# Optimization experiments

Hardware: AMD Instinct MI355X
Metric: run time of the kernel (lower is better)

## Reference

```python
import jax, jax.numpy as jnp
import numpy as np

NUM_HEADS = 16
EMBED_DIM = 1024
LN_EPS = 1e-5


def setup_inputs() -> dict:
    key = jax.random.key(0)
    ks = jax.random.split(key, 9)
    B, S, D = 4, 1024, EMBED_DIM
    return {
        "query": jax.random.normal(ks[0], (B, S, D), dtype=jnp.float32),
        "key": jax.random.normal(ks[1], (B, S, D), dtype=jnp.float32),
        "value": jax.random.normal(ks[2], (B, S, D), dtype=jnp.float32),
        "W_query": 0.01 * jax.random.normal(ks[3], (D, D), dtype=jnp.float32),
        "W_key": 0.01 * jax.random.normal(ks[4], (D, D), dtype=jnp.float32),
        "W_value": 0.01 * jax.random.normal(ks[5], (D, D), dtype=jnp.float32),
        "W_output": 0.01 * jax.random.normal(ks[6], (D, D), dtype=jnp.float32),
        "ln_gamma": jnp.ones((D,), dtype=jnp.float32),
        "ln_beta": jnp.zeros((D,), dtype=jnp.float32),
        "mask": 1,
    }


def _split_heads(x):
    # [B,S,D] -> [H,B,S,d]; torch split(dim=-1)+stack(dim=0) gives head h = cols h*d:(h+1)*d
    B, S, D = x.shape
    d = D // NUM_HEADS
    return jnp.moveaxis(x.reshape(B, S, NUM_HEADS, d), 2, 0)


def reference(query, key, value, W_query, W_key, W_value, W_output, ln_gamma, ln_beta, mask):
    B, S, D = query.shape
    d = D // NUM_HEADS
    q = _split_heads(query @ W_query)   # [H,B,S,d]
    k = _split_heads(key @ W_key)       # [H,B,S,d]
    v = _split_heads(value @ W_value)   # [H,B,S,d]
    scale = jnp.asarray(np.sqrt(d), dtype=q.dtype)
    scores = jnp.einsum("hbqd,hbkd->hbqk", q, k) / scale  # [H,B,S,S]
    attn = jax.nn.softmax(scores, axis=-1)
    if mask:
        # post-hoc causal: zero strict upper triangle, then renormalize rows
        tri = jnp.tril(jnp.ones((S, S), dtype=bool))
        attn = jnp.where(tri, attn, 0.0)
        attn = attn / jnp.sum(attn, axis=-1, keepdims=True)
    ws = jnp.einsum("hbqk,hbkd->hbqd", attn, v)            # [H,B,S,d]
    concat = jnp.moveaxis(ws, 0, 2).reshape(B, S, D)       # [B,S,D]
    out = concat @ W_output + query                        # residual
    mu = jnp.mean(out, axis=-1, keepdims=True)
    var = jnp.var(out, axis=-1, keepdims=True)
    out = (out - mu) / jnp.sqrt(var + LN_EPS) * ln_gamma + ln_beta
    return out, attn
```

## Files before the change

kernel.cpp:

```cpp
#include <hip/hip_runtime.h>
#include <hip/hip_bf16.h>

#define Bn   4
#define Sn   1024
#define Dn   1024
#define Hn   16
#define dHn  64
#define HB   (Hn * Bn)
#define MROWS (Bn * Sn)
#define QNE  ((size_t)Bn * Sn * Dn)

typedef __attribute__((ext_vector_type(8))) short bf16x8;
typedef __attribute__((ext_vector_type(4))) float f32x4;

__device__ __forceinline__ ushort f2bf(float x) {
  union { float f; unsigned u; } v; v.f = x;
  unsigned r = v.u + 0x7FFF + ((v.u >> 16) & 1);
  return (ushort)(r >> 16);
}
__device__ __forceinline__ float bf2f(ushort u) {
  union { unsigned u; float f; } v; v.u = ((unsigned)u) << 16; return v.f;
}

__device__ __forceinline__ void load_lds16(const void* g, void* l) {
  __builtin_amdgcn_global_load_lds(
      (const __attribute__((address_space(1))) unsigned int*)g,
      (__attribute__((address_space(3))) unsigned int*)l, 16, 0, 0);
}

__global__ __launch_bounds__(256) void cast3_kernel(
    const float* __restrict__ q, const float* __restrict__ k,
    const float* __restrict__ v, ushort* __restrict__ outb) {
  const float* in = blockIdx.y == 0 ? q : (blockIdx.y == 1 ? k : v);
  ushort* out = outb + (size_t)blockIdx.y * QNE;
  int idx = blockIdx.x * 256 + threadIdx.x;
  float4 x = *(const float4*)&in[(size_t)idx * 4];
  ushort4 o;
  o.x = f2bf(x.x); o.y = f2bf(x.y); o.z = f2bf(x.z); o.w = f2bf(x.w);
  *(ushort4*)&out[(size_t)idx * 4] = o;
}

__global__ __launch_bounds__(256) void transpose4_kernel(
    const float* __restrict__ Wq, const float* __restrict__ Wk,
    const float* __restrict__ Wv, const float* __restrict__ Wo,
    ushort* __restrict__ WTb) {
  const int z = blockIdx.z;
  const float* W = z == 0 ? Wq : (z == 1 ? Wk : (z == 2 ? Wv : Wo));
  ushort* WT = WTb + (size_t)z * Dn * Dn;
  __shared__ ushort T[64 * 72];
  const int k0 = blockIdx.y * 64, n0 = blockIdx.x * 64;
  const int t = threadIdx.x;
  const int r = t >> 4, c4 = (t & 15) * 4;
#pragma unroll
  for (int i = 0; i < 4; ++i) {
    int row = r + i * 16;
    float4 v = *(const float4*)&W[(size_t)(k0 + row) * Dn + n0 + c4];
    T[(c4 + 0) * 72 + row] = f2bf(v.x);
    T[(c4 + 1) * 72 + row] = f2bf(v.y);
    T[(c4 + 2) * 72 + row] = f2bf(v.z);
    T[(c4 + 3) * 72 + row] = f2bf(v.w);
  }
  __syncthreads();
#pragma unroll
  for (int i = 0; i < 2; ++i) {
    int c = t + i * 256;
    int n = c >> 3, kg = (c & 7) * 8;
    *(ulonglong2*)&WT[(size_t)(n0 + n) * Dn + k0 + kg] =
        *(const ulonglong2*)&T[n * 72 + kg];
  }
}

__global__ __launch_bounds__(256, 3) void qkv_gemm(
    const ushort* __restrict__ Ab, const ushort* __restrict__ Bb,
    ushort* __restrict__ Cb) {
  const int z = blockIdx.z;
  const ushort* A  = Ab + (size_t)z * QNE;
  const ushort* Bt = Bb + (size_t)z * Dn * Dn;
  ushort* C        = Cb + (size_t)z * QNE;
  const int N = Dn, K = Dn;

  __shared__ ushort lds[17408];
  ushort* As = lds;
  ushort* Bs = lds + 4096;
  const int t = threadIdx.x;
  const int w = t >> 6, lane = t & 63;
  const int wr = (w >> 1) * 64, wc = (w & 1) * 64;
  const int l16 = lane & 15, quad = lane >> 4;
  const int flat = blockIdx.y * 8 + blockIdx.x;
  const int nf = (flat & 7) * 32 + (flat >> 3);
  const int m0 = (nf >> 3) * 128, n0 = (nf & 7) * 128;
  const int srow = (lane >> 2);
  const int scol = (lane & 3) * 8;
  f32x4 acc[4][4] = {};
  for (int k0 = 0; k0 < K; k0 += 32) {
#pragma unroll
    for (int c = 0; c < 2; ++c) {
      int row = w * 32 + c * 16 + srow;
      load_lds16(&A[(size_t)(m0 + row) * K + k0 + scol],
                 &As[(size_t)w * 1024 + c * 512]);
      load_lds16(&Bt[(size_t)(n0 + row) * K + k0 + scol],
                 &Bs[(size_t)w * 1024 + c * 512]);
    }
    __syncthreads();
    bf16x8 af[4], bfr[4];
#pragma unroll
    for (int mi = 0; mi < 4; ++mi)
      af[mi] = *(const bf16x8*)&As[(wr + mi * 16 + l16) * 32 + quad * 8];
#pragma unroll
    for (int ni = 0; ni < 4; ++ni)
      bfr[ni] = *(const bf16x8*)&Bs[(wc + ni * 16 + l16) * 32 + quad * 8];
#pragma unroll
    for (int mi = 0; mi < 4; ++mi)
#pragma unroll
      for (int ni = 0; ni < 4; ++ni)
        acc[mi][ni] = __builtin_amdgcn_mfma_f32_16x16x32_bf16(
            af[mi], bfr[ni], acc[mi][ni], 0, 0, 0);
    __syncthreads();
  }
  if (z == 2) {
    ushort* Cs = lds;
#pragma unroll
    for (int mi = 0; mi < 4; ++mi)
#pragma unroll
      for (int ni = 0; ni < 4; ++ni) {
        int col = wc + ni * 16 + l16;
#pragma unroll
        for (int r = 0; r < 4; ++r)
          Cs[col * 136 + wr + mi * 16 + quad * 4 + r] = f2bf(acc[mi][ni][r]);
      }
    __syncthreads();
    const int b = m0 >> 10, s0 = m0 & 1023;
#pragma unroll
    for (int i = 0; i < 8; ++i) {
      int c = t + i * 256;
      int nl = c >> 4, mg = (c & 15) * 8;
      *(ulonglong2*)&C[((size_t)b * Dn + n0 + nl) * Sn + s0 + mg] =
          *(const ulonglong2*)&Cs[nl * 136 + mg];
    }
  } else {
    ushort* Cs = lds;
#pragma unroll
    for (int mi = 0; mi < 4; ++mi)
#pragma unroll
      for (int ni = 0; ni < 4; ++ni) {
        int col = wc + ni * 16 + l16;
#pragma unroll
        for (int r = 0; r < 4; ++r)
          Cs[(wr + mi * 16 + quad * 4 + r) * 136 + col] = f2bf(acc[mi][ni][r]);
      }
    __syncthreads();
#pragma unroll
    for (int i = 0; i < 8; ++i) {
      int c = t + i * 256;
      int row = c >> 4, cg = (c & 15) * 8;
      *(ulonglong2*)&C[(size_t)(m0 + row) * N + n0 + cg] =
          *(const ulonglong2*)&Cs[row * 136 + cg];
    }
  }
}

__global__ __launch_bounds__(256, 3) void gemm_out(
    const ushort* __restrict__ A, const ushort* __restrict__ Bt,
    const float* __restrict__ resid, float* __restrict__ C,
    int M, int N, int K) {
  __shared__ ushort lds[6144];
  ushort* As = lds;
  ushort* Bs = lds + 4096;
  const int t = threadIdx.x;
  const int w = t >> 6, lane = t & 63;
  const int wr = (w >> 1) * 64, wc = (w & 1) * 32;
  const int l16 = lane & 15, quad = lane >> 4;
  const int f = blockIdx.y * 16 + blockIdx.x;
  const int idx = f >> 3;
  const int m0 = ((f & 7) * 4 + (idx >> 4)) * 128;
  const int n0 = (idx & 15) * 64;
  const int srow = (lane >> 2);
  const int scol = (lane & 3) * 8;
  f32x4 acc[4][2] = {};
  for (int k0 = 0; k0 < K; k0 += 32) {
#pragma unroll
    for (int c = 0; c < 2; ++c) {
      int row = w * 32 + c * 16 + srow;
      load_lds16(&A[(size_t)(m0 + row) * K + k0 + scol],
                 &As[(size_t)w * 1024 + c * 512]);
    }
    load_lds16(&Bt[(size_t)(n0 + w * 16 + srow) * K + k0 + scol],
               &Bs[(size_t)w * 512]);
    __syncthreads();
    bf16x8 af[4], bfr[2];
#pragma unroll
    for (int mi = 0; mi < 4; ++mi)
      af[mi] = *(const bf16x8*)&As[(wr + mi * 16 + l16) * 32 + quad * 8];
#pragma unroll
    for (int ni = 0; ni < 2; ++ni)
      bfr[ni] = *(const bf16x8*)&Bs[(wc + ni * 16 + l16) * 32 + quad * 8];
#pragma unroll
    for (int mi = 0; mi < 4; ++mi)
#pragma unroll
      for (int ni = 0; ni < 2; ++ni)
        acc[mi][ni] = __builtin_amdgcn_mfma_f32_16x16x32_bf16(
            af[mi], bfr[ni], acc[mi][ni], 0, 0, 0);
    __syncthreads();
  }
#pragma unroll
  for (int mi = 0; mi < 4; ++mi)
#pragma unroll
    for (int ni = 0; ni < 2; ++ni) {
      int n = n0 + wc + ni * 16 + l16;
#pragma unroll
      for (int r = 0; r < 4; ++r) {
        int m = m0 + wr + mi * 16 + quad * 4 + r;
        float v = acc[mi][ni][r];
        v += resid[(size_t)m * N + n];
        C[(size_t)m * N + n] = v;
      }
    }
}

__global__ __launch_bounds__(256, 3) void attn_fused(
    const ushort* __restrict__ Qp, const ushort* __restrict__ Kp,
    const ushort* __restrict__ Vt, ushort* __restrict__ Pu,
    float* __restrict__ attn, ushort* __restrict__ Cc) {
  const int hb = blockIdx.x, qt = (gridDim.y - 1) - blockIdx.y;
  const int h = hb >> 2, b = hb & 3;
  const int q0 = qt * 64;
  const int nkt = (qt >> 1) + 1;

  __shared__ ushort lds[9216 + 8704];
  ushort* Ks = lds;
  ushort* Ps = lds + 9216;
  ushort* Vs = lds;
  __shared__ float lds_inv[64];

  const int t = threadIdx.x;
  const int w = t >> 6, lane = t & 63;
  const int l16 = lane & 15, quad = lane >> 4;

  for (int ktz = nkt; ktz < 8; ++ktz) {
    const int k0 = ktz * 128;
#pragma unroll
    for (int i = 0; i < 4; ++i) {
      int cc = t + i * 256;
      int row = cc >> 4, cg = (cc & 15) * 8;
      float* dst = &attn[((size_t)hb * Sn + q0 + row) * Sn + k0 + cg];
      *(float4*)&dst[0] = make_float4(0.f, 0.f, 0.f, 0.f);
      *(float4*)&dst[4] = make_float4(0.f, 0.f, 0.f, 0.f);
    }
  }

  bf16x8 aq[2];
#pragma unroll
  for (int ks = 0; ks < 2; ++ks)
    aq[ks] = *(const bf16x8*)&Qp[((size_t)b * Sn + q0 + w * 16 + l16) * Dn +
                                 h * dHn + ks * 32 + quad * 8];

  float l_run[4] = {0.f, 0.f, 0.f, 0.f};

  for (int kt = 0; kt < nkt; ++kt) {
    const int k0 = kt * 128;
    const bool halfT = (kt == nkt - 1) && ((qt & 1) == 0);
    const int nni = halfT ? 4 : 8;
    const int kiters = halfT ? 2 : 4;
#pragma unroll
    for (int i = 0; i < 4; ++i) {
      if (i < kiters) {
        int cc = t + i * 256;
        int row = cc >> 3, cg = (cc & 7) * 8;
        *(ulonglong2*)&Ks[row * 72 + cg] =
            *(const ulonglong2*)&Kp[((size_t)b * Sn + k0 + row) * Dn + h * dHn + cg];
      }
    }
    __syncthreads();
    f32x4 s[8];
#pragma unroll
    for (int ni = 0; ni < 8; ++ni) {
      if (ni < nni) {
        f32x4 a = {};
#pragma unroll
        for (int ks = 0; ks < 2; ++ks) {
          bf16x8 bk = *(const bf16x8*)&Ks[(ni * 16 + l16) * 72 + ks * 32 + quad * 8];
          a = __builtin_amdgcn_mfma_f32_16x16x32_bf16(aq[ks], bk, a, 0, 0, 0);
        }
        s[ni] = a;
      }
    }
    float tsum[4] = {0.f, 0.f, 0.f, 0.f};
#pragma unroll
    for (int ni = 0; ni < 8; ++ni)
#pragma unroll
      for (int r = 0; r < 4; ++r) {
        int dst = (w * 16 + quad * 4 + r) * 136 + ni * 16 + l16;
        if (ni < nni) {
          int kg = k0 + ni * 16 + l16;
          int qg = q0 + w * 16 + quad * 4 + r;
          float v = (kg <= qg) ? s[ni][r] * 0.125f : -3e38f;
          float p = __expf(v);
          tsum[r] += p;
          Ps[dst] = f2bf(p);
        } else {
          Ps[dst] = (ushort)0;
        }
      }
#pragma unroll
    for (int d = 1; d < 16; d <<= 1)
#pragma unroll
      for (int r = 0; r < 4; ++r) tsum[r] += __shfl_xor(tsum[r], d);
#pragma unroll
    for (int r = 0; r < 4; ++r) l_run[r] += tsum[r];
    __syncthreads();
#pragma unroll
    for (int i = 0; i < 4; ++i) {
      int cc = t + i * 256;
      int row = cc >> 4, cg = (cc & 15) * 8;
      *(ulonglong2*)&Pu[((size_t)hb * Sn + q0 + row) * Sn + k0 + cg] =
          *(const ulonglong2*)&Ps[row * 136 + cg];
    }
  }
  float inv_l[4];
#pragma unroll
  for (int r = 0; r < 4; ++r) inv_l[r] = 1.0f / l_run[r];
  if (l16 == 0)
#pragma unroll
    for (int r = 0; r < 4; ++r) lds_inv[w * 16 + quad * 4 + r] = inv_l[r];
  __syncthreads();

  f32x4 acc_o[4] = {};
  for (int kt = 0; kt < nkt; ++kt) {
    const int k0 = kt * 128;
    const bool halfT = (kt == nkt - 1) && ((qt & 1) == 0);
    const int nks = halfT ? 2 : 4;
    if (halfT) {
#pragma unroll
      for (int i = 0; i < 2; ++i) {
        int cc = t + i * 256;
        int row = cc >> 3, cg = (cc & 7) * 8;
        *(ulonglong2*)&Vs[row * 136 + cg] =
            *(const ulonglong2*)&Vt[((size_t)b * Dn + h * dHn + row) * Sn + k0 + cg];
      }
    } else {
#pragma unroll
      for (int i = 0; i < 4; ++i) {
        int cc = t + i * 256;
        int row = cc >> 4, cg = (cc & 15) * 8;
        *(ulonglong2*)&Vs[row * 136 + cg] =
            *(const ulonglong2*)&Vt[((size_t)b * Dn + h * dHn + row) * Sn + k0 + cg];
      }
    }
    __syncthreads();
#pragma unroll
    for (int ks = 0; ks < 4; ++ks) {
      if (ks < nks) {
        bf16x8 ap = *(const bf16x8*)&Pu[((size_t)hb * Sn + q0 + w * 16 + l16) * Sn +
                                        k0 + ks * 32 + quad * 8];
#pragma unroll
        for (int ni = 0; ni < 4; ++ni) {
          bf16x8 bv = *(const bf16x8*)&Vs[(ni * 16 + l16) * 136 + ks * 32 + quad * 8];
          acc_o[ni] = __builtin_amdgcn_mfma_f32_16x16x32_bf16(ap, bv, acc_o[ni], 0, 0, 0);
        }
      }
    }
#pragma unroll
    for (int i = 0; i < 4; ++i) {
      int cc = t + i * 256;
      int row = cc >> 4, cg = (cc & 15) * 8;
      float inv = lds_inv[row];
      bf16x8 pv = *(const bf16x8*)&Pu[((size_t)hb * Sn + q0 + row) * Sn + k0 + cg];
      float* dst = &attn[((size_t)hb * Sn + q0 + row) * Sn + k0 + cg];
      *(float4*)&dst[0] = make_float4(bf2f((ushort)pv[0]) * inv, bf2f((ushort)pv[1]) * inv,
                                      bf2f((ushort)pv[2]) * inv, bf2f((ushort)pv[3]) * inv);
      *(float4*)&dst[4] = make_float4(bf2f((ushort)pv[4]) * inv, bf2f((ushort)pv[5]) * inv,
                                      bf2f((ushort)pv[6]) * inv, bf2f((ushort)pv[7]) * inv);
    }
    __syncthreads();
  }
#pragma unroll
  for (int ni = 0; ni < 4; ++ni)
#pragma unroll
    for (int r = 0; r < 4; ++r) {
      int q = q0 + w * 16 + quad * 4 + r;
      int j = ni * 16 + l16;
      Cc[((size_t)b * Sn + q) * Dn + h * dHn + j] = f2bf(acc_o[ni][r] * inv_l[r]);
    }
}

__global__ __launch_bounds__(256) void ln_kernel(
    float* __restrict__ out, const float* __restrict__ gamma,
    const float* __restrict__ beta) {
  const int row = blockIdx.x;
  float* p = out + (size_t)row * Dn;
  const int t = threadIdx.x;
  float4 x = *(const float4*)&p[t * 4];
  float s  = x.x + x.y + x.z + x.w;
  float s2 = x.x * x.x + x.y * x.y + x.z * x.z + x.w * x.w;
#pragma unroll
  for (int d = 1; d < 64; d <<= 1) {
    s  += __shfl_xor(s, d);
    s2 += __shfl_xor(s2, d);
  }
  __shared__ float a1[4], a2[4];
  const int w = t >> 6, lane = t & 63;
  if (lane == 0) { a1[w] = s; a2[w] = s2; }
  __syncthreads();
  s  = a1[0] + a1[1] + a1[2] + a1[3];
  s2 = a2[0] + a2[1] + a2[2] + a2[3];
  const float mu  = s * (1.0f / Dn);
  const float var = s2 * (1.0f / Dn) - mu * mu;
  const float rstd = rsqrtf(var + 1e-5f);
  float4 g  = *(const float4*)&gamma[t * 4];
  float4 be = *(const float4*)&beta[t * 4];
  float4 o;
  o.x = (x.x - mu) * rstd * g.x + be.x;
  o.y = (x.y - mu) * rstd * g.y + be.y;
  o.z = (x.z - mu) * rstd * g.z + be.z;
  o.w = (x.w - mu) * rstd * g.w + be.w;
  *(float4*)&p[t * 4] = o;
}

extern "C" void kernel_launch(void* const* d_in, const int* in_sizes, int n_in,
                              void* d_out, int out_size, void* d_ws, size_t ws_size,
                              hipStream_t stream) {
  const float* q_in  = (const float*)d_in[0];
  const float* k_in  = (const float*)d_in[1];
  const float* v_in  = (const float*)d_in[2];
  const float* Wq    = (const float*)d_in[3];
  const float* Wk    = (const float*)d_in[4];
  const float* Wv    = (const float*)d_in[5];
  const float* Wo    = (const float*)d_in[6];
  const float* gamma = (const float*)d_in[7];
  const float* beta  = (const float*)d_in[8];

  float* out  = (float*)d_out;
  float* attn = out + (size_t)Bn * Sn * Dn;

  ushort* ws  = (ushort*)d_ws;
  ushort* qbf = ws;
  ushort* kbf = qbf + QNE;
  ushort* vbf = kbf + QNE;
  ushort* WqT = vbf + QNE;
  ushort* WkT = WqT + (size_t)Dn * Dn;
  ushort* WvT = WkT + (size_t)Dn * Dn;
  ushort* WoT = WvT + (size_t)Dn * Dn;
  ushort* Qp  = WoT + (size_t)Dn * Dn;
  ushort* Kp  = Qp + QNE;
  ushort* Vt  = Kp + QNE;
  ushort* Cc  = Vt + QNE;
  ushort* Pu  = Cc + QNE;

  (void)kbf; (void)vbf; (void)WkT; (void)WvT; (void)Kp;

  cast3_kernel<<<dim3(QNE / 1024, 3), 256, 0, stream>>>(q_in, k_in, v_in, qbf);
  transpose4_kernel<<<dim3(Dn / 64, Dn / 64, 4), 256, 0, stream>>>(Wq, Wk, Wv, Wo, WqT);

  qkv_gemm<<<dim3(Dn / 128, MROWS / 128, 3), 256, 0, stream>>>(qbf, WqT, Qp);

  attn_fused<<<dim3(HB, Sn / 64), 256, 0, stream>>>(Qp, Kp, Vt, Pu, attn, Cc);

  gemm_out<<<dim3(Dn / 64, MROWS / 128), 256, 0, stream>>>(Cc, WoT, q_in, out, MROWS, Dn, Dn);
  ln_kernel<<<MROWS, 256, 0, stream>>>(out, gamma, beta);
}
```

Before: 472.9 us.

## Recompute QK^T in second attention pass instead of spilling P to global

The first pass now only accumulates row sums of the exponentiated scores. The second pass reloads K, recomputes QK^T and exp into an LDS P tile, and uses it for both PV and the normalized attention write. This removes the bf16 P scratch buffer round-trip through global memory. In exchange it doubles the QK^T MFMA and exp work and adds K loads, and the split LDS arrays raise shared memory use, which may lower occupancy.

```diff
diff --git a/kernel.cpp b/kernel.cpp
--- a/kernel.cpp
+++ b/kernel.cpp
@@ -219,17 +219,16 @@
 
 __global__ __launch_bounds__(256, 3) void attn_fused(
     const ushort* __restrict__ Qp, const ushort* __restrict__ Kp,
-    const ushort* __restrict__ Vt, ushort* __restrict__ Pu,
-    float* __restrict__ attn, ushort* __restrict__ Cc) {
+    const ushort* __restrict__ Vt, float* __restrict__ attn,
+    ushort* __restrict__ Cc) {
   const int hb = blockIdx.x, qt = (gridDim.y - 1) - blockIdx.y;
   const int h = hb >> 2, b = hb & 3;
   const int q0 = qt * 64;
   const int nkt = (qt >> 1) + 1;
 
-  __shared__ ushort lds[9216 + 8704];
-  ushort* Ks = lds;
-  ushort* Ps = lds + 9216;
-  ushort* Vs = lds;
+  __shared__ ushort Ks[128 * 72];
+  __shared__ ushort Vs[64 * 136];
+  __shared__ ushort Ps[64 * 136];
   __shared__ float lds_inv[64];
 
   const int t = threadIdx.x;
@@ -286,21 +285,16 @@
     }
     float tsum[4] = {0.f, 0.f, 0.f, 0.f};
 #pragma unroll
-    for (int ni = 0; ni < 8; ++ni)
-#pragma unroll
-      for (int r = 0; r < 4; ++r) {
-        int dst = (w * 16 + quad * 4 + r) * 136 + ni * 16 + l16;
-        if (ni < nni) {
+    for (int ni = 0; ni < 8; ++ni) {
+      if (ni < nni)
+#pragma unroll
+        for (int r = 0; r < 4; ++r) {
           int kg = k0 + ni * 16 + l16;
           int qg = q0 + w * 16 + quad * 4 + r;
-          float v = (kg <= qg) ? s[ni][r] * 0.125f : -3e38f;
-          float p = __expf(v);
-          tsum[r] += p;
-          Ps[dst] = f2bf(p);
-        } else {
-          Ps[dst] = (ushort)0;
+          float e = __expf(s[ni][r] * 0.125f);
+          tsum[r] += (kg <= qg) ? e : 0.f;
         }
-      }
+    }
 #pragma unroll
     for (int d = 1; d < 16; d <<= 1)
 #pragma unroll
@@ -308,13 +302,6 @@
 #pragma unroll
     for (int r = 0; r < 4; ++r) l_run[r] += tsum[r];
     __syncthreads();
-#pragma unroll
-    for (int i = 0; i < 4; ++i) {
-      int cc = t + i * 256;
-      int row = cc >> 4, cg = (cc & 15) * 8;
-      *(ulonglong2*)&Pu[((size_t)hb * Sn + q0 + row) * Sn + k0 + cg] =
-          *(const ulonglong2*)&Ps[row * 136 + cg];
-    }
   }
   float inv_l[4];
 #pragma unroll
@@ -328,7 +315,18 @@
   for (int kt = 0; kt < nkt; ++kt) {
     const int k0 = kt * 128;
     const bool halfT = (kt == nkt - 1) && ((qt & 1) == 0);
+    const int nni = halfT ? 4 : 8;
+    const int kiters = halfT ? 2 : 4;
     const int nks = halfT ? 2 : 4;
+#pragma unroll
+    for (int i = 0; i < 4; ++i) {
+      if (i < kiters) {
+        int cc = t + i * 256;
+        int row = cc >> 3, cg = (cc & 7) * 8;
+        *(ulonglong2*)&Ks[row * 72 + cg] =
+            *(const ulonglong2*)&Kp[((size_t)b * Sn + k0 + row) * Dn + h * dHn + cg];
+      }
+    }
     if (halfT) {
 #pragma unroll
       for (int i = 0; i < 2; ++i) {
@@ -347,11 +345,37 @@
       }
     }
     __syncthreads();
+    f32x4 s[8];
+#pragma unroll
+    for (int ni = 0; ni < 8; ++ni) {
+      if (ni < nni) {
+        f32x4 a = {};
+#pragma unroll
+        for (int ks = 0; ks < 2; ++ks) {
+          bf16x8 bk = *(const bf16x8*)&Ks[(ni * 16 + l16) * 72 + ks * 32 + quad * 8];
+          a = __builtin_amdgcn_mfma_f32_16x16x32_bf16(aq[ks], bk, a, 0, 0, 0);
+        }
+        s[ni] = a;
+      }
+    }
+#pragma unroll
+    for (int ni = 0; ni < 8; ++ni)
+#pragma unroll
+      for (int r = 0; r < 4; ++r) {
+        int pd = (w * 16 + quad * 4 + r) * 136 + ni * 16 + l16;
+        float p = 0.f;
+        if (ni < nni) {
+          int kg = k0 + ni * 16 + l16;
+          int qg = q0 + w * 16 + quad * 4 + r;
+          float e = __expf(s[ni][r] * 0.125f);
+          p = (kg <= qg) ? e : 0.f;
+        }
+        Ps[pd] = f2bf(p);
+      }
 #pragma unroll
     for (int ks = 0; ks < 4; ++ks) {
       if (ks < nks) {
-        bf16x8 ap = *(const bf16x8*)&Pu[((size_t)hb * Sn + q0 + w * 16 + l16) * Sn +
-                                        k0 + ks * 32 + quad * 8];
+        bf16x8 ap = *(const bf16x8*)&Ps[(w * 16 + l16) * 136 + ks * 32 + quad * 8];
 #pragma unroll
         for (int ni = 0; ni < 4; ++ni) {
           bf16x8 bv = *(const bf16x8*)&Vs[(ni * 16 + l16) * 136 + ks * 32 + quad * 8];
@@ -359,19 +383,19 @@
         }
       }
     }
+    __syncthreads();
 #pragma unroll
     for (int i = 0; i < 4; ++i) {
       int cc = t + i * 256;
       int row = cc >> 4, cg = (cc & 15) * 8;
       float inv = lds_inv[row];
-      bf16x8 pv = *(const bf16x8*)&Pu[((size_t)hb * Sn + q0 + row) * Sn + k0 + cg];
+      bf16x8 pv = *(const bf16x8*)&Ps[row * 136 + cg];
       float* dst = &attn[((size_t)hb * Sn + q0 + row) * Sn + k0 + cg];
       *(float4*)&dst[0] = make_float4(bf2f((ushort)pv[0]) * inv, bf2f((ushort)pv[1]) * inv,
                                       bf2f((ushort)pv[2]) * inv, bf2f((ushort)pv[3]) * inv);
       *(float4*)&dst[4] = make_float4(bf2f((ushort)pv[4]) * inv, bf2f((ushort)pv[5]) * inv,
                                       bf2f((ushort)pv[6]) * inv, bf2f((ushort)pv[7]) * inv);
     }
-    __syncthreads();
   }
 #pragma unroll
   for (int ni = 0; ni < 4; ++ni)
@@ -444,7 +468,6 @@
   ushort* Kp  = Qp + QNE;
   ushort* Vt  = Kp + QNE;
   ushort* Cc  = Vt + QNE;
-  ushort* Pu  = Cc + QNE;
 
   (void)kbf; (void)vbf; (void)WkT; (void)WvT; (void)Kp;
 
@@ -453,7 +476,7 @@
 
   qkv_gemm<<<dim3(Dn / 128, MROWS / 128, 3), 256, 0, stream>>>(qbf, WqT, Qp);
 
-  attn_fused<<<dim3(HB, Sn / 64), 256, 0, stream>>>(Qp, Kp, Vt, Pu, attn, Cc);
+  attn_fused<<<dim3(HB, Sn / 64), 256, 0, stream>>>(Qp, Kp, Vt, attn, Cc);
 
   gemm_out<<<dim3(Dn / 64, MROWS / 128), 256, 0, stream>>>(Cc, WoT, q_in, out, MROWS, Dn, Dn);
   ln_kernel<<<MROWS, 256, 0, stream>>>(out, gamma, beta);
```

New measurement: 445.6 us. -5.8%, faster.
